# Optimization experiments

Hardware: AMD Instinct MI355X
Metric: run time of the kernel (lower is better)

## Reference

```python
import jax, jax.numpy as jnp
import numpy as np

# Constants from the module's __init__ (LIFNodes / RUMNodes / Connection args)
DT = 1.0
TAU = 10.0            # LIF membrane time constant
TC_TRACE = 20.0       # spike-trace time constant (bindsnet default)
REST, RESET, THRESH = -70.0, -65.0, -55.0
ALPHA, BETA = 0.95, 0.8     # RUM hidden leak / threshold-adaptation decay
H_THRESH = 1.0              # hidden firing threshold
NU1_PRE, NU1_POST = 0.001, 0.01    # PostPre STDP rates (input->hidden)
NU2 = 0.0001                        # MSTDP learning rate (hidden->output)
WMIN, WMAX = 0.0, 1.0
REWARD = 1.0
A_PLUS, A_MINUS = 1.0, -1.0         # MSTDP trace amplitudes (bindsnet defaults)
TC_PM = 20.0                        # MSTDP p_plus/p_minus time constant
INPUT_GAIN = 20.0   # scales U[0,1) rates into the LIF operating range (rest->thresh gap = 15 mV)

IN_D, HID_D, OUT_D = 544, 1024, 2048


def setup_inputs() -> dict:
    key = jax.random.key(0)
    k1, k2, k3 = jax.random.split(key, 3)
    x = jax.random.uniform(k1, (IN_D,), dtype=jnp.float32)            # rate-coded input
    w1 = jax.random.uniform(k2, (IN_D, HID_D), dtype=jnp.float32)     # in [wmin, wmax]
    w2 = jax.random.uniform(k3, (HID_D, OUT_D), dtype=jnp.float32)
    return {"x": x, "w1": w1, "w2": w2, "num_timesteps": 500}


def _simulate(x, w1, w2, T):
    decay_v = jnp.float32(np.exp(-DT / TAU))
    decay_tr = jnp.float32(np.exp(-DT / TC_TRACE))
    decay_pm = jnp.float32(np.exp(-DT / TC_PM))
    rates = x * INPUT_GAIN  # constant input current each timestep (rate coding)

    carry = (
        jnp.full((IN_D,), REST, jnp.float32),   # v_in
        jnp.zeros((HID_D,), jnp.float32),        # v_hid
        jnp.full((OUT_D,), REST, jnp.float32),   # v_out
        jnp.zeros((IN_D,), jnp.float32),         # tr_in  (pre trace, PostPre)
        jnp.zeros((HID_D,), jnp.float32),        # tr_hid (post trace, PostPre)
        jnp.zeros((HID_D,), jnp.float32),        # b_hid  (RUM threshold adaptation)
        jnp.zeros((HID_D,), jnp.float32),        # p_plus  (MSTDP pre trace)
        jnp.zeros((OUT_D,), jnp.float32),        # p_minus (MSTDP post trace)
        w1, w2,
    )

    def step(c, _):
        v_in, v_hid, v_out, tr_in, tr_hid, b_hid, p_plus, p_minus, w1c, w2c = c
        # --- input LIF: decay toward rest, integrate rates, spike, reset ---
        v_in = decay_v * (v_in - REST) + REST + rates
        s_in = (v_in >= THRESH).astype(jnp.float32)
        v_in = jnp.where(s_in > 0, RESET, v_in)
        tr_in = jnp.where(s_in > 0, 1.0, tr_in * decay_tr)
        # --- hidden RUM: leaky integration (alpha) + adaptive threshold (beta) ---
        i_hid = s_in @ w1c                                  # [HID]
        v_hid = ALPHA * v_hid + i_hid
        s_hid = (v_hid >= H_THRESH + b_hid).astype(jnp.float32)
        v_hid = jnp.where(s_hid > 0, 0.0, v_hid)
        b_hid = BETA * b_hid + s_hid
        tr_hid_new = jnp.where(s_hid > 0, 1.0, tr_hid * decay_tr)
        # --- output LIF ---
        i_out = s_hid @ w2c                                 # [OUT]
        v_out = decay_v * (v_out - REST) + REST + i_out
        s_out = (v_out >= THRESH).astype(jnp.float32)
        v_out = jnp.where(s_out > 0, RESET, v_out)
        # --- PostPre STDP on w1: potentiate on post spike, depress on pre spike ---
        w1c = jnp.clip(
            w1c + NU1_POST * jnp.outer(tr_in, s_hid) - NU1_PRE * jnp.outer(s_in, tr_hid_new),
            WMIN, WMAX)
        # --- MSTDP on w2: reward-modulated eligibility ---
        p_plus = decay_pm * p_plus + A_PLUS * s_hid
        p_minus = decay_pm * p_minus + A_MINUS * s_out
        elig = jnp.outer(p_plus, s_out) + jnp.outer(s_hid, p_minus)  # [HID, OUT]
        w2c = w2c + NU2 * REWARD * DT * elig
        new_c = (v_in, v_hid, v_out, tr_in, tr_hid_new, b_hid, p_plus, p_minus, w1c, w2c)
        return new_c, s_out

    _, spikes = jax.lax.scan(step, carry, None, length=T)
    return spikes  # [T, OUT_D] float32 spike raster (== stacked monitor recording)


def reference(x, w1, w2, num_timesteps):
    return _simulate(x, w1, w2, num_timesteps)
```

## Files before the change

kernel.cpp:

```cpp
#include <hip/hip_runtime.h>
#include <stdint.h>


#define DECAY_V  0.90483741803595952f
#define DECAY_TR 0.95122942450071403f
#define REST_F   (-70.0f)
#define RESET_F  (-65.0f)
#define THRESH_F (-55.0f)
#define ALPHA_F  (0.95f)
#define BETA_F   (0.8f)
#define NU1_PRE_F  (0.001f)
#define NU1_POST_F (0.01f)
#define NU2_F      (0.0001f)
#define GAIN_F     (20.0f)
#define LOG2D    (-0.072134752044448170f)

static constexpr int IN_D  = 544;
static constexpr int HID_D = 1024;
static constexpr int OUT_D = 2048;
static constexpr int TMAX  = 512;

#define DP1  0.95122942450071403f
#define DP2  0.90483741803595957f
#define DP4  0.81873075307798186f
#define DP8  0.67032004603563930f
#define DP16 0.44932896411722159f
#define DP32 0.20189651799465541f

__device__ __forceinline__ float rdlane(float x, int l) {
    return __builtin_bit_cast(float,
        __builtin_amdgcn_readlane(__builtin_bit_cast(int, x), l));
}

template <int CTRL>
__device__ __forceinline__ float dpp_add(float x) {
    int y = __builtin_amdgcn_update_dpp(0, __builtin_bit_cast(int, x),
                                        CTRL, 0xF, 0xF, true);
    return x + __builtin_bit_cast(float, y);
}

__device__ __forceinline__ float wave_sum64(float x) {
    x = dpp_add<0xB1>(x);
    x = dpp_add<0x4E>(x);
    x = dpp_add<0x114>(x);
    x = dpp_add<0x118>(x);
    x = dpp_add<0x142>(x);
    x = dpp_add<0x143>(x);
    return rdlane(x, 63);
}

__global__ __launch_bounds__(256, 2)
void hidden_kernel(const float* __restrict__ x, const float* __restrict__ w1,
                   const int* __restrict__ Tp, float* __restrict__ Sf)
{
    const int T = Tp[0];
    const int tid = threadIdx.x, lane = tid & 63, wv = tid >> 6;
    const int cp = wv >> 1;
    const int h  = wv & 1;
    const int col = blockIdx.x * 2 + cp;
    const float c0 = REST_F * (1.0f - DECAY_V);
    __shared__ float part[2][4];

    float w[5], vi[5], tr[5], cadd[5];
    #pragma unroll
    for (int k = 0; k < 5; ++k) {
        const int o = 64 * k + lane;
        const int i = 272 * h + o;
        const bool ok = (o < 272);
        w[k]    = ok ? w1[(size_t)i * HID_D + col] : 0.f;
        cadd[k] = c0 + (ok ? x[i] * GAIN_F : 0.f);
        vi[k]   = REST_F;
        tr[k]   = 0.f;
    }
    float v_h = 0.f, b_h = 0.f, tr_h = 0.f;
    const bool writer = (h == 0 && lane == 0);

    auto step = [&](int t, int par) {
        float acc = 0.f, s[5];
        #pragma unroll
        for (int k = 0; k < 5; ++k) {
            const float vv = fmaf(DECAY_V, vi[k], cadd[k]);
            const bool sp = (vv >= THRESH_F);
            vi[k] = sp ? RESET_F : vv;
            s[k]  = sp ? 1.f : 0.f;
            tr[k] = fmaxf(tr[k] * DECAY_TR, s[k]);
            acc   = fmaf(s[k], w[k], acc);
        }
        const float p = wave_sum64(acc);
        if (lane == 0) part[par][wv] = p;
        __syncthreads();
        const float tot = p + part[par][wv ^ 1];
        const float vh2 = fmaf(ALPHA_F, v_h, tot);
        const bool hp = (vh2 >= 1.0f + b_h);
        const float sh = hp ? 1.f : 0.f;
        v_h  = hp ? 0.f : vh2;
        b_h  = fmaf(BETA_F, b_h, sh);
        tr_h = hp ? 1.f : tr_h * DECAY_TR;
        const float apot = hp ? NU1_POST_F : 0.f;
        const float adep = NU1_PRE_F * tr_h;
        #pragma unroll
        for (int k = 0; k < 5; ++k) {
            const float a  = fmaf(apot, tr[k], w[k]);
            const float nw = fmaf(-adep, s[k], a);
            w[k] = __builtin_amdgcn_fmed3f(nw, 0.f, 1.f);
        }
        if (writer) Sf[(size_t)t * HID_D + col] = sh;
    };

    int t = 0;
    for (; t + 1 < T; t += 2) {
        step(t, 0);
        step(t + 1, 1);
    }
    if (t < T) step(t, 0);
}

__global__ void pack_kernel(float* __restrict__ Sf, const int* __restrict__ Tp,
                            unsigned long long* __restrict__ Sb)
{
    const int T = Tp[0];
    const int t = blockIdx.x;
    const int lane = threadIdx.x & 63, wv = threadIdx.x >> 6;
    if (t >= T) {
        ((float4*)(Sf + (size_t)t * HID_D))[threadIdx.x] = make_float4(0.f, 0.f, 0.f, 0.f);
        return;
    }
    #pragma unroll
    for (int q = 0; q < 4; ++q) {
        const int word = wv * 4 + q;
        const float s = Sf[(size_t)t * HID_D + word * 64 + lane];
        const unsigned long long m = __ballot(s > 0.5f);
        if (lane == 0) Sb[(size_t)t * 16 + word] = m;
    }
}

__global__ __launch_bounds__(256)
void gramgemm_kernel(const unsigned long long* __restrict__ Sb,
                     const int* __restrict__ Tp, float* __restrict__ G,
                     const float* __restrict__ Sf, const float* __restrict__ w2,
                     float* __restrict__ AT, int klen)
{
    __shared__ __align__(16) char smem[16640];
    const int b = blockIdx.x, tid = threadIdx.x;
    if (b < 1024) {
        const int by = b >> 5, bx = b & 31;
        if (bx > by) return;
        const int T = Tp[0];
        typedef unsigned long long u64;
        u64 (*tR)[17] = (u64(*)[17])(smem);
        u64 (*uR)[17] = (u64(*)[17])(smem + 2176);
        {
            const int r = tid >> 4, w0 = tid & 15;
            const int trow = by * 16 + r, urow = bx * 16 + r;
            tR[r][w0] = (trow < T) ? Sb[(size_t)trow * 16 + w0] : 0ULL;
            uR[r][w0] = (urow < T) ? Sb[(size_t)urow * 16 + w0] : 0ULL;
        }
        __syncthreads();
        const int tx = tid & 15, ty = tid >> 4;
        const int t = by * 16 + ty, u = bx * 16 + tx;
        if (t < T && u < t) {
            int s = 0;
            #pragma unroll
            for (int w0 = 0; w0 < 16; ++w0) s += __popcll(tR[ty][w0] & uR[tx][w0]);
            G[(size_t)t * TMAX + u] = (float)s;
        }
    } else {
        const int g = b - 1024;
        const int z = g >> 7, r = g & 127;
        const int j0 = (r & 15) * 128, t0 = (r >> 4) * 64;
        const int kbase = z * klen;
        float (*Ss)[68]  = (float(*)[68])(smem);
        float (*Ws)[192] = (float(*)[192])(smem + 4352);
        const int sr = tid >> 2, sq = tid & 3;
        const int wq2 = tid & 31, wr2 = tid >> 5;
        const int wcol = (wq2 >> 1) * 12 + (wq2 & 1) * 4;
        const int tj = tid & 15, tt = tid >> 4;
        const int tjc = tj * 12;

        float acc[4][8];
        #pragma unroll
        for (int a = 0; a < 4; ++a)
            #pragma unroll
            for (int bb = 0; bb < 8; ++bb) acc[a][bb] = 0.f;

        for (int k0 = 0; k0 < klen; k0 += 16) {
            const float4 sv = *(const float4*)&Sf[(size_t)(t0 + sr) * HID_D + kbase + k0 + sq * 4];
            const float4 wa = *(const float4*)&w2[(size_t)(kbase + k0 + wr2) * OUT_D + j0 + wq2 * 4];
            const float4 wb = *(const float4*)&w2[(size_t)(kbase + k0 + wr2 + 8) * OUT_D + j0 + wq2 * 4];
            __syncthreads();
            Ss[sq * 4 + 0][sr] = sv.x;
            Ss[sq * 4 + 1][sr] = sv.y;
            Ss[sq * 4 + 2][sr] = sv.z;
            Ss[sq * 4 + 3][sr] = sv.w;
            *(float4*)&Ws[wr2][wcol] = wa;
            *(float4*)&Ws[wr2 + 8][wcol] = wb;
            __syncthreads();
            #pragma unroll
            for (int kk = 0; kk < 16; ++kk) {
                const float4 a4 = *(const float4*)&Ss[kk][tt * 4];
                const float4 b0 = *(const float4*)&Ws[kk][tjc];
                const float4 b1 = *(const float4*)&Ws[kk][tjc + 4];
                const float aa[4] = {a4.x, a4.y, a4.z, a4.w};
                const float bbv[8] = {b0.x, b0.y, b0.z, b0.w, b1.x, b1.y, b1.z, b1.w};
                #pragma unroll
                for (int ti = 0; ti < 4; ++ti)
                    #pragma unroll
                    for (int jj = 0; jj < 8; ++jj)
                        acc[ti][jj] = fmaf(aa[ti], bbv[jj], acc[ti][jj]);
            }
        }
        #pragma unroll
        for (int jj = 0; jj < 8; ++jj)
            *(float4*)&AT[(size_t)z * OUT_D * TMAX +
                          (size_t)(j0 + tj * 8 + jj) * TMAX + t0 + tt * 4] =
                make_float4(acc[0][jj], acc[1][jj], acc[2][jj], acc[3][jj]);
    }
}

__global__ __launch_bounds__(256)
void mt_kernel(const float* __restrict__ G, const int* __restrict__ Tp,
               float* __restrict__ MT)
{
    const int T = Tp[0];
    const int lane = threadIdx.x & 63;
    const int t = blockIdx.x * 4 + (threadIdx.x >> 6);
    if (t >= T) return;
    const float* Gr = G + (size_t)t * TMAX;
    const float dl1  = exp2f((float)(lane + 1) * LOG2D);
    const float d64l = exp2f((float)(64 - lane) * LOG2D);

    float g[8], kk[8];
    #pragma unroll
    for (int c = 0; c < 8; ++c) {
        const int tau = 64 * c + lane;
        g[c] = (tau < t) ? Gr[tau] : 0.f;
    }
    float kc = 0.f;
    #pragma unroll
    for (int c = 7; c >= 0; --c) {
        float k = g[c], u;
        u = __shfl_down(k, 1, 64);  if (lane < 63) k = fmaf(DP1, u, k);
        u = __shfl_down(k, 2, 64);  if (lane < 62) k = fmaf(DP2, u, k);
        u = __shfl_down(k, 4, 64);  if (lane < 60) k = fmaf(DP4, u, k);
        u = __shfl_down(k, 8, 64);  if (lane < 56) k = fmaf(DP8, u, k);
        u = __shfl_down(k, 16, 64); if (lane < 48) k = fmaf(DP16, u, k);
        u = __shfl_down(k, 32, 64); if (lane < 32) k = fmaf(DP32, u, k);
        k = fmaf(d64l, kc, k);
        kk[c] = k;
        kc = rdlane(k, 0);
    }
    float hc = 0.f;
    #pragma unroll
    for (int c = 0; c < 8; ++c) {
        float h = g[c], u;
        u = __shfl_up(h, 1, 64);  if (lane >= 1)  h = fmaf(DP1, u, h);
        u = __shfl_up(h, 2, 64);  if (lane >= 2)  h = fmaf(DP2, u, h);
        u = __shfl_up(h, 4, 64);  if (lane >= 4)  h = fmaf(DP4, u, h);
        u = __shfl_up(h, 8, 64);  if (lane >= 8)  h = fmaf(DP8, u, h);
        u = __shfl_up(h, 16, 64); if (lane >= 16) h = fmaf(DP16, u, h);
        u = __shfl_up(h, 32, 64); if (lane >= 32) h = fmaf(DP32, u, h);
        h = fmaf(dl1, hc, h);
        const int tau = 64 * c + lane;
        if (tau < t) MT[(size_t)tau * TMAX + t] = NU2_F * (h - kk[c]);
        hc = rdlane(h, 63);
    }
}

template <int C>
__device__ __forceinline__ void out_chunk(
    const float* __restrict__ AT, const float* __restrict__ MT,
    float (&hs)[4][8], float (&v)[4],
    float* __restrict__ out, int j, int lane, int T, int nparts,
    float* __restrict__ LD, float4* __restrict__ so4)
{
    const int rem = T - 64 * C;
    const int mtv = (rem < 64) ? rem : 64;
    float av[4];
    #pragma unroll
    for (int q = 0; q < 4; ++q) {
        float a = AT[(size_t)(j + q) * TMAX + 64 * C + lane];
        for (int p = 1; p < nparts; ++p)
            a += AT[(size_t)p * OUT_D * TMAX + (size_t)(j + q) * TMAX + 64 * C + lane];
        av[q] = a;
    }
    const float* ldb = LD + (C & 1) * 4096;
    float acc[4];
    #pragma unroll
    for (int q = 0; q < 4; ++q) acc[q] = hs[q][C];
    float mv0 = ldb[lane];
    float mv1 = (mtv > 1) ? ldb[64 + lane] : 0.f;
    for (int tt = 0; tt < mtv; ++tt) {
        const float mv = mv0;
        mv0 = mv1;
        if (tt + 2 < mtv) mv1 = ldb[(tt + 2) * 64 + lane];
        float so[4];
        #pragma unroll
        for (int q = 0; q < 4; ++q) {
            const float iv = rdlane(av[q] + acc[q], tt);
            const float vd = fmaf(DECAY_V, v[q], REST_F * (1.0f - DECAY_V)) + iv;
            const bool sp = (vd >= THRESH_F);
            so[q] = sp ? 1.f : 0.f;
            v[q]  = sp ? RESET_F : vd;
        }
        if (lane == 0)
            *(float4*)&out[(size_t)(64 * C + tt) * OUT_D + j] =
                make_float4(so[0], so[1], so[2], so[3]);
        if (lane == tt) so4[tt] = make_float4(so[0], so[1], so[2], so[3]);
        #pragma unroll
        for (int q = 0; q < 4; ++q) acc[q] = fmaf(so[q], mv, acc[q]);
    }
    if (C + 1 < 8 && 64 * (C + 1) < T) {
        {
            float* dst = LD + ((C + 1) & 1) * 4096;
            const float* src = MT + (size_t)(64 * (C + 1)) * TMAX + 64 * (C + 1) + lane;
            #pragma unroll 16
            for (int rr = 0; rr < 64; ++rr) {
                const float vv = src[(size_t)rr * TMAX];
                dst[rr * 64 + lane] = (rr < lane) ? vv : 0.f;
            }
        }
        for (int tt = 0; tt < mtv; ++tt) {
            const float4 s = so4[tt];
            const float* Mrow = MT + (size_t)(64 * C + tt) * TMAX + lane;
            #pragma unroll
            for (int K = C + 1; K < 8; ++K) {
                const float mval = Mrow[64 * K];
                hs[0][K] = fmaf(s.x, mval, hs[0][K]);
                hs[1][K] = fmaf(s.y, mval, hs[1][K]);
                hs[2][K] = fmaf(s.z, mval, hs[2][K]);
                hs[3][K] = fmaf(s.w, mval, hs[3][K]);
            }
        }
    }
}

__global__ __launch_bounds__(64, 2)
void out_kernel(const float* __restrict__ AT, const float* __restrict__ MT,
                const int* __restrict__ Tp, float* __restrict__ out, int nparts)
{
    const int T = Tp[0];
    const int lane = threadIdx.x;
    const int j = blockIdx.x * 4;
    __shared__ float LD[2 * 4096];
    __shared__ float4 so4[64];

    float hs[4][8];
    #pragma unroll
    for (int q = 0; q < 4; ++q)
        #pragma unroll
        for (int k = 0; k < 8; ++k) hs[q][k] = 0.f;
    float v[4] = {REST_F, REST_F, REST_F, REST_F};

    {
        const float* src = MT + lane;
        #pragma unroll 16
        for (int rr = 0; rr < 64; ++rr) {
            const float vv = src[(size_t)rr * TMAX];
            LD[rr * 64 + lane] = (rr < lane) ? vv : 0.f;
        }
    }
    out_chunk<0>(AT, MT, hs, v, out, j, lane, T, nparts, LD, so4);
    if (T >  64) out_chunk<1>(AT, MT, hs, v, out, j, lane, T, nparts, LD, so4);
    if (T > 128) out_chunk<2>(AT, MT, hs, v, out, j, lane, T, nparts, LD, so4);
    if (T > 192) out_chunk<3>(AT, MT, hs, v, out, j, lane, T, nparts, LD, so4);
    if (T > 256) out_chunk<4>(AT, MT, hs, v, out, j, lane, T, nparts, LD, so4);
    if (T > 320) out_chunk<5>(AT, MT, hs, v, out, j, lane, T, nparts, LD, so4);
    if (T > 384) out_chunk<6>(AT, MT, hs, v, out, j, lane, T, nparts, LD, so4);
    if (T > 448) out_chunk<7>(AT, MT, hs, v, out, j, lane, T, nparts, LD, so4);
}

extern "C" void kernel_launch(void* const* d_in, const int* in_sizes, int n_in,
                              void* d_out, int out_size, void* d_ws, size_t ws_size,
                              hipStream_t stream) {
    const float* x  = (const float*)d_in[0];
    const float* w1 = (const float*)d_in[1];
    const float* w2 = (const float*)d_in[2];
    const int*   Tp = (const int*)d_in[3];
    float* out = (float*)d_out;
    char* ws = (char*)d_ws;
    unsigned long long* Sb = (unsigned long long*)(ws);
    float* G  = (float*)(ws + 65536);
    float* MT = (float*)(ws + 65536 + 1048576);
    float* Sf = (float*)(ws + 65536 + 2 * 1048576);
    float* AT = (float*)(ws + 65536 + 4 * 1048576);
    const size_t base  = 65536 + 4 * 1048576;
    const int nparts = (ws_size >= base + 4 * 4194304) ? 4
                     : (ws_size >= base + 2 * 4194304) ? 2 : 1;
    const int klen = 1024 / nparts;

    hipLaunchKernelGGL(hidden_kernel, dim3(HID_D / 2), dim3(256), 0, stream, x, w1, Tp, Sf);
    hipLaunchKernelGGL(pack_kernel,   dim3(TMAX), dim3(256), 0, stream, Sf, Tp, Sb);
    hipLaunchKernelGGL(gramgemm_kernel, dim3(1024 + 128 * nparts), dim3(256), 0, stream,
                       Sb, Tp, G, Sf, w2, AT, klen);
    hipLaunchKernelGGL(mt_kernel,     dim3(128), dim3(256), 0, stream, G, Tp, MT);
    hipLaunchKernelGGL(out_kernel,    dim3(OUT_D / 4), dim3(64), 0, stream, AT, MT, Tp, out, nparts);
}
```

Before: 343.2 us.

## Split out_kernel columns across four wavefronts sharing cooperatively loaded MT tiles

The output kernel now runs 256 threads per block, with each 64-lane wavefront handling one output neuron instead of one wavefront serially handling four. The triangular MT tile for the next chunk is loaded cooperatively (16 rows per wave) before the current chunk's sequential scan. Spikes are kept in a per-lane register and written once per chunk rather than through a float4 LDS buffer. The steady-state loop is manually unrolled by four with a rotating prefetch of M values. This shortens each wave's serial dependency chain and raises parallelism, in exchange for a __syncthreads per chunk and four times more MT global reads for the hs update, since each wave now streams those rows separately.

```diff
diff --git a/kernel.cpp b/kernel.cpp
--- a/kernel.cpp
+++ b/kernel.cpp
@@ -269,104 +269,116 @@
 template <int C>
 __device__ __forceinline__ void out_chunk(
     const float* __restrict__ AT, const float* __restrict__ MT,
-    float (&hs)[4][8], float (&v)[4],
-    float* __restrict__ out, int j, int lane, int T, int nparts,
-    float* __restrict__ LD, float4* __restrict__ so4)
-{
-    const int rem = T - 64 * C;
+    float (&hs)[8], float& v, float* __restrict__ out,
+    int j, int lane, int w, int T, int nparts, float* __restrict__ LD)
+{
+    __syncthreads();
+    constexpr int t0 = 64 * C;
+    const int rem = T - t0;
     const int mtv = (rem < 64) ? rem : 64;
-    float av[4];
-    #pragma unroll
-    for (int q = 0; q < 4; ++q) {
-        float a = AT[(size_t)(j + q) * TMAX + 64 * C + lane];
-        for (int p = 1; p < nparts; ++p)
-            a += AT[(size_t)p * OUT_D * TMAX + (size_t)(j + q) * TMAX + 64 * C + lane];
-        av[q] = a;
+    float av = AT[(size_t)j * TMAX + t0 + lane];
+    #pragma unroll
+    for (int p = 1; p < 4; ++p)
+        if (p < nparts)
+            av += AT[(size_t)p * OUT_D * TMAX + (size_t)j * TMAX + t0 + lane];
+    const bool hasNext = (C + 1 < 8) && (64 * (C + 1) < T);
+    if (hasNext) {
+        float* dst = LD + ((C + 1) & 1) * 4096;
+        const float* src = MT + (size_t)(64 * (C + 1)) * TMAX + 64 * (C + 1) + lane;
+        #pragma unroll
+        for (int rr = 0; rr < 16; ++rr) {
+            const int r = w * 16 + rr;
+            const float vv = src[(size_t)r * TMAX];
+            dst[r * 64 + lane] = (r < lane) ? vv : 0.f;
+        }
     }
     const float* ldb = LD + (C & 1) * 4096;
-    float acc[4];
-    #pragma unroll
-    for (int q = 0; q < 4; ++q) acc[q] = hs[q][C];
-    float mv0 = ldb[lane];
-    float mv1 = (mtv > 1) ? ldb[64 + lane] : 0.f;
-    for (int tt = 0; tt < mtv; ++tt) {
-        const float mv = mv0;
-        mv0 = mv1;
-        if (tt + 2 < mtv) mv1 = ldb[(tt + 2) * 64 + lane];
-        float so[4];
-        #pragma unroll
-        for (int q = 0; q < 4; ++q) {
-            const float iv = rdlane(av[q] + acc[q], tt);
-            const float vd = fmaf(DECAY_V, v[q], REST_F * (1.0f - DECAY_V)) + iv;
+    const float cc = REST_F * (1.0f - DECAY_V);
+    float acc = hs[C];
+    float sreg = 0.f;
+
+    auto sstep = [&](int tt, float& m, int reload) {
+        const float iv = rdlane(av + acc, tt);
+        const float vd = fmaf(DECAY_V, v, cc) + iv;
+        const bool sp = (vd >= THRESH_F);
+        const float so = sp ? 1.f : 0.f;
+        v = sp ? RESET_F : vd;
+        sreg = (lane == tt) ? so : sreg;
+        acc = fmaf(so, m, acc);
+        if (reload < 64) m = ldb[reload * 64 + lane];
+    };
+
+    if (rem >= 64) {
+        float m0 = ldb[lane], m1 = ldb[64 + lane],
+              m2 = ldb[128 + lane], m3 = ldb[192 + lane];
+        #pragma unroll 1
+        for (int tt = 0; tt < 64; tt += 4) {
+            sstep(tt,     m0, tt + 4);
+            sstep(tt + 1, m1, tt + 5);
+            sstep(tt + 2, m2, tt + 6);
+            sstep(tt + 3, m3, tt + 7);
+        }
+    } else {
+        float m0 = ldb[lane];
+        float m1 = (mtv > 1) ? ldb[64 + lane] : 0.f;
+        for (int tt = 0; tt < mtv; ++tt) {
+            const float mv = m0;
+            m0 = m1;
+            if (tt + 2 < mtv) m1 = ldb[(tt + 2) * 64 + lane];
+            const float iv = rdlane(av + acc, tt);
+            const float vd = fmaf(DECAY_V, v, cc) + iv;
             const bool sp = (vd >= THRESH_F);
-            so[q] = sp ? 1.f : 0.f;
-            v[q]  = sp ? RESET_F : vd;
-        }
-        if (lane == 0)
-            *(float4*)&out[(size_t)(64 * C + tt) * OUT_D + j] =
-                make_float4(so[0], so[1], so[2], so[3]);
-        if (lane == tt) so4[tt] = make_float4(so[0], so[1], so[2], so[3]);
-        #pragma unroll
-        for (int q = 0; q < 4; ++q) acc[q] = fmaf(so[q], mv, acc[q]);
-    }
-    if (C + 1 < 8 && 64 * (C + 1) < T) {
-        {
-            float* dst = LD + ((C + 1) & 1) * 4096;
-            const float* src = MT + (size_t)(64 * (C + 1)) * TMAX + 64 * (C + 1) + lane;
-            #pragma unroll 16
-            for (int rr = 0; rr < 64; ++rr) {
-                const float vv = src[(size_t)rr * TMAX];
-                dst[rr * 64 + lane] = (rr < lane) ? vv : 0.f;
-            }
-        }
-        for (int tt = 0; tt < mtv; ++tt) {
-            const float4 s = so4[tt];
-            const float* Mrow = MT + (size_t)(64 * C + tt) * TMAX + lane;
+            const float so = sp ? 1.f : 0.f;
+            v = sp ? RESET_F : vd;
+            sreg = (lane == tt) ? so : sreg;
+            acc = fmaf(so, mv, acc);
+        }
+    }
+    if (lane < mtv) out[(size_t)(t0 + lane) * OUT_D + j] = sreg;
+
+    if (hasNext) {
+        #pragma unroll 4
+        for (int tt = 0; tt < 64; ++tt) {
+            const float s = rdlane(sreg, tt);
+            const float* Mrow = MT + (size_t)(t0 + tt) * TMAX + lane;
             #pragma unroll
-            for (int K = C + 1; K < 8; ++K) {
-                const float mval = Mrow[64 * K];
-                hs[0][K] = fmaf(s.x, mval, hs[0][K]);
-                hs[1][K] = fmaf(s.y, mval, hs[1][K]);
-                hs[2][K] = fmaf(s.z, mval, hs[2][K]);
-                hs[3][K] = fmaf(s.w, mval, hs[3][K]);
-            }
-        }
-    }
-}
-
-__global__ __launch_bounds__(64, 2)
+            for (int K = C + 1; K < 8; ++K)
+                hs[K] = fmaf(s, Mrow[64 * K], hs[K]);
+        }
+    }
+}
+
+__global__ __launch_bounds__(256, 2)
 void out_kernel(const float* __restrict__ AT, const float* __restrict__ MT,
                 const int* __restrict__ Tp, float* __restrict__ out, int nparts)
 {
     const int T = Tp[0];
-    const int lane = threadIdx.x;
-    const int j = blockIdx.x * 4;
+    const int tid = threadIdx.x, lane = tid & 63, w = tid >> 6;
+    const int j = blockIdx.x * 4 + w;
     __shared__ float LD[2 * 4096];
-    __shared__ float4 so4[64];
-
-    float hs[4][8];
-    #pragma unroll
-    for (int q = 0; q < 4; ++q)
-        #pragma unroll
-        for (int k = 0; k < 8; ++k) hs[q][k] = 0.f;
-    float v[4] = {REST_F, REST_F, REST_F, REST_F};
+
+    float hs[8];
+    #pragma unroll
+    for (int k = 0; k < 8; ++k) hs[k] = 0.f;
+    float v = REST_F;
 
     {
         const float* src = MT + lane;
-        #pragma unroll 16
-        for (int rr = 0; rr < 64; ++rr) {
-            const float vv = src[(size_t)rr * TMAX];
-            LD[rr * 64 + lane] = (rr < lane) ? vv : 0.f;
-        }
-    }
-    out_chunk<0>(AT, MT, hs, v, out, j, lane, T, nparts, LD, so4);
-    if (T >  64) out_chunk<1>(AT, MT, hs, v, out, j, lane, T, nparts, LD, so4);
-    if (T > 128) out_chunk<2>(AT, MT, hs, v, out, j, lane, T, nparts, LD, so4);
-    if (T > 192) out_chunk<3>(AT, MT, hs, v, out, j, lane, T, nparts, LD, so4);
-    if (T > 256) out_chunk<4>(AT, MT, hs, v, out, j, lane, T, nparts, LD, so4);
-    if (T > 320) out_chunk<5>(AT, MT, hs, v, out, j, lane, T, nparts, LD, so4);
-    if (T > 384) out_chunk<6>(AT, MT, hs, v, out, j, lane, T, nparts, LD, so4);
-    if (T > 448) out_chunk<7>(AT, MT, hs, v, out, j, lane, T, nparts, LD, so4);
+        #pragma unroll
+        for (int rr = 0; rr < 16; ++rr) {
+            const int r = w * 16 + rr;
+            const float vv = src[(size_t)r * TMAX];
+            LD[r * 64 + lane] = (r < lane) ? vv : 0.f;
+        }
+    }
+    out_chunk<0>(AT, MT, hs, v, out, j, lane, w, T, nparts, LD);
+    if (T >  64) out_chunk<1>(AT, MT, hs, v, out, j, lane, w, T, nparts, LD);
+    if (T > 128) out_chunk<2>(AT, MT, hs, v, out, j, lane, w, T, nparts, LD);
+    if (T > 192) out_chunk<3>(AT, MT, hs, v, out, j, lane, w, T, nparts, LD);
+    if (T > 256) out_chunk<4>(AT, MT, hs, v, out, j, lane, w, T, nparts, LD);
+    if (T > 320) out_chunk<5>(AT, MT, hs, v, out, j, lane, w, T, nparts, LD);
+    if (T > 384) out_chunk<6>(AT, MT, hs, v, out, j, lane, w, T, nparts, LD);
+    if (T > 448) out_chunk<7>(AT, MT, hs, v, out, j, lane, w, T, nparts, LD);
 }
 
 extern "C" void kernel_launch(void* const* d_in, const int* in_sizes, int n_in,
@@ -393,5 +405,5 @@
     hipLaunchKernelGGL(gramgemm_kernel, dim3(1024 + 128 * nparts), dim3(256), 0, stream,
                        Sb, Tp, G, Sf, w2, AT, klen);
     hipLaunchKernelGGL(mt_kernel,     dim3(128), dim3(256), 0, stream, G, Tp, MT);
-    hipLaunchKernelGGL(out_kernel,    dim3(OUT_D / 4), dim3(64), 0, stream, AT, MT, Tp, out, nparts);
-}
+    hipLaunchKernelGGL(out_kernel,    dim3(OUT_D / 4), dim3(256), 0, stream, AT, MT, Tp, out, nparts);
+}
```

Measured after the change: 275.4 us. 19.8% less time.
